# Kernel optimization log

Measured on AMD Instinct MI355X. Metric: run time of the kernel, lower is better.

The kernel has to match this reference:

```python
import jax, jax.numpy as jnp
import numpy as np

N, E_SC, E_BB = 50000, 600000, 100000
D, ED, REMB, NRES, SBF = 128, 128, 32, 21, 16
PI = 3.14159


def ln(x, g, b):
    m = jnp.mean(x, -1, keepdims=True)
    v = jnp.mean((x - m) ** 2, -1, keepdims=True)
    return (x - m) * jax.lax.rsqrt(v + 1e-5) * g + b


def gcn(x, W, b, src, dst, w):
    # GCNConv: symmetric normalization with unit self-loops and edge weights w.
    n = x.shape[0]
    xw = x @ W
    deg = jax.ops.segment_sum(w, dst, num_segments=n) + 1.0  # +1 self-loop
    dis = jax.lax.rsqrt(jnp.maximum(deg, 1e-6))  # clamp: hat_e.mean can be negative
    norm = dis[src] * w * dis[dst]
    agg = jax.ops.segment_sum(norm[:, None] * xw[src], dst, num_segments=n)
    return agg + (dis * dis)[:, None] * xw + b


def core(V_com, SBF_chi, X_c_alpha, V_c_beta, SBF_phi, SBF_psi, d_sidechain_com, d_min,
         old_chi, old_phi, old_psi, old_cbeta_coords, old_calpha_coords,
         res_table, sc_ln_g, sc_ln_b, sc_W, sc_b, bb_ln_g, bb_ln_b, bb_W, bb_b,
         e_ln_g, e_ln_b, eW1, eb1, eW2, eb2, euW, eub, gW, gb, bgW, bgb,
         iW1, ib1, iW2, ib2, aW, ab, baW, bab, cW, cb, xW, xb,
         residue_idx_i, residue_idx_j, edge_index_sc, edge_index_bb):
    hat_h = ln(jnp.concatenate([V_com, SBF_chi], -1), sc_ln_g, sc_ln_b) @ sc_W + sc_b
    h = ln(jnp.concatenate([X_c_alpha, V_c_beta, SBF_phi, SBF_psi], -1), bb_ln_g, bb_ln_b) @ bb_W + bb_b
    pair = jnp.concatenate([res_table[residue_idx_i], res_table[residue_idx_j]], -1)
    e_in = jnp.concatenate([d_sidechain_com[:, None], d_min[:, None], pair], -1)
    hat_e = jax.nn.relu(ln(e_in, e_ln_g, e_ln_b) @ eW1 + eb1) @ eW2 + eb2
    src, dst = edge_index_sc[0], edge_index_sc[1]
    for _ in range(3):  # num_sidechain_layers
        w = hat_e.mean(-1)
        hat_h = hat_h + jax.nn.relu(gcn(hat_h, gW, gb, src, dst, w))
        hat_e = hat_e + jnp.concatenate([hat_h[src], hat_h[dst]], -1) @ euW + eub
    bsrc, bdst = edge_index_bb[0], edge_index_bb[1]
    ebb = jnp.ones(bsrc.shape[0], hat_h.dtype)
    for _ in range(2):
        m = jax.nn.relu(jnp.concatenate([h, hat_h], -1) @ iW1 + ib1) @ iW2 + ib2
        h = h + jax.nn.relu(gcn(h, bgW, bgb, bsrc, bdst, ebb)) + m
    sc_act = jax.nn.relu(hat_h)
    bb_act = jax.nn.relu(h)
    wrap = lambda a: (a + PI) % (2.0 * PI) - PI
    dchi = (sc_act @ aW + ab)[:, 0]
    chi_new = wrap(old_chi + dchi[None, :])  # [4, N]
    dphi = (bb_act @ baW + bab)[:, 0]
    phi_new = wrap(old_phi + dphi)
    psi_new = wrap(old_psi + dphi)  # same bb_angle_head applied twice in source
    V_cbeta_new = old_cbeta_coords + sc_act @ cW + cb
    X_calpha_new = old_calpha_coords + bb_act @ xW + xb
    return chi_new, phi_new, psi_new, V_cbeta_new, X_calpha_new


def setup_inputs() -> dict:
    key = jax.random.key(0)
    ks = jax.random.split(key, 40)
    rn = lambda i, s: jax.random.normal(ks[i], s, jnp.float32)
    p = lambda i, s: rn(i, s) * 0.05
    return dict(
        V_com=rn(0, (N, 3)), SBF_chi=rn(1, (N, SBF)), X_c_alpha=rn(2, (N, 3)),
        V_c_beta=rn(3, (N, 3)), SBF_phi=rn(4, (N, SBF)), SBF_psi=rn(5, (N, SBF)),
        d_sidechain_com=jax.random.uniform(ks[6], (E_SC,), jnp.float32),
        d_min=jax.random.uniform(ks[7], (E_SC,), jnp.float32),
        old_chi=rn(8, (4, N)), old_phi=rn(9, (N,)), old_psi=rn(10, (N,)),
        old_cbeta_coords=rn(11, (N, 3)), old_calpha_coords=rn(12, (N, 3)),
        res_table=p(13, (NRES, REMB)),
        sc_ln_g=jnp.ones(3 + SBF), sc_ln_b=jnp.zeros(3 + SBF), sc_W=p(14, (3 + SBF, D)), sc_b=jnp.zeros(D),
        bb_ln_g=jnp.ones(6 + 2 * SBF), bb_ln_b=jnp.zeros(6 + 2 * SBF), bb_W=p(15, (6 + 2 * SBF, D)), bb_b=jnp.zeros(D),
        e_ln_g=jnp.ones(2 + 2 * REMB), e_ln_b=jnp.zeros(2 + 2 * REMB),
        eW1=p(16, (2 + 2 * REMB, ED)), eb1=jnp.zeros(ED), eW2=p(17, (ED, ED)), eb2=jnp.zeros(ED),
        euW=p(18, (2 * D, ED)), eub=jnp.zeros(ED),
        gW=p(19, (D, D)), gb=jnp.zeros(D), bgW=p(20, (D, D)), bgb=jnp.zeros(D),
        iW1=p(21, (2 * D, D)), ib1=jnp.zeros(D), iW2=p(22, (D, D)), ib2=jnp.zeros(D),
        aW=p(23, (D, 1)), ab=jnp.zeros(1), baW=p(24, (D, 1)), bab=jnp.zeros(1),
        cW=p(25, (D, 3)), cb=jnp.zeros(3), xW=p(26, (D, 3)), xb=jnp.zeros(3),
        residue_idx_i=jax.random.randint(ks[27], (E_SC,), 0, NRES),
        residue_idx_j=jax.random.randint(ks[28], (E_SC,), 0, NRES),
        edge_index_sc=jax.random.randint(ks[29], (2, E_SC), 0, N),
        edge_index_bb=jax.random.randint(ks[30], (2, E_BB), 0, N),
    )


def reference(V_com, SBF_chi, X_c_alpha, V_c_beta, SBF_phi, SBF_psi, d_sidechain_com, d_min,
              old_chi, old_phi, old_psi, old_cbeta_coords, old_calpha_coords,
              res_table, sc_ln_g, sc_ln_b, sc_W, sc_b, bb_ln_g, bb_ln_b, bb_W, bb_b,
              e_ln_g, e_ln_b, eW1, eb1, eW2, eb2, euW, eub, gW, gb, bgW, bgb,
              iW1, ib1, iW2, ib2, aW, ab, baW, bab, cW, cb, xW, xb,
              residue_idx_i, residue_idx_j, edge_index_sc, edge_index_bb):
    return core(V_com, SBF_chi, X_c_alpha, V_c_beta, SBF_phi, SBF_psi, d_sidechain_com, d_min,
                old_chi, old_phi, old_psi, old_cbeta_coords, old_calpha_coords,
                res_table, sc_ln_g, sc_ln_b, sc_W, sc_b, bb_ln_g, bb_ln_b, bb_W, bb_b,
                e_ln_g, e_ln_b, eW1, eb1, eW2, eb2, euW, eub, gW, gb, bgW, bgb,
                iW1, ib1, iW2, ib2, aW, ab, baW, bab, cW, cb, xW, xb,
                residue_idx_i, residue_idx_j, edge_index_sc, edge_index_bb)
```

## Files before the change

### kernel.cpp

```cpp
#include <hip/hip_runtime.h>
#include <stdint.h>

#define DEVI __device__ __forceinline__

constexpr int N_   = 50000;
constexpr int ESC  = 600000;
constexpr int EBB  = 100000;
constexpr int NRES = 21;
constexpr float PI_F = 3.14159f;

constexpr int RCH = 2048;
constexpr int RBS = (ESC + RCH - 1)/RCH;
constexpr int RBB = (EBB + RCH - 1)/RCH;

typedef __attribute__((ext_vector_type(8))) short short8v;
typedef __attribute__((ext_vector_type(4))) float f32x4;

DEVI float bf2f(unsigned short u){ return __uint_as_float(((unsigned)u)<<16); }
DEVI unsigned short f2bf(float f){
  unsigned x = __float_as_uint(f);
  unsigned r = (x + 0x7FFFu + ((x>>16)&1u))>>16;
  return (unsigned short)r;
}
DEVI float ldin(const void* p, long i, int f32){
  return f32 ? ((const float*)p)[i] : bf2f(((const unsigned short*)p)[i]);
}
DEVI void stout(void* p, long i, float v, int f32){
  if(f32) ((float*)p)[i]=v; else ((unsigned short*)p)[i]=f2bf(v);
}
DEVI float wrapf(float a){
  float t = a + PI_F;
  const float TP = 2.f*PI_F;
  t -= floorf(t/TP)*TP;
  return t - PI_F;
}

constexpr int OW_SC_LN_G=0;
constexpr int OW_SC_LN_B=OW_SC_LN_G+19;
constexpr int OW_SC_W  = OW_SC_LN_B+19;
constexpr int OW_SC_B  = OW_SC_W+19*128;
constexpr int OW_BB_LN_G=OW_SC_B+128;
constexpr int OW_BB_LN_B=OW_BB_LN_G+38;
constexpr int OW_BB_W = OW_BB_LN_B+38;
constexpr int OW_BB_B = OW_BB_W+38*128;
constexpr int OW_E_LN_G=OW_BB_B+128;
constexpr int OW_E_LN_B=OW_E_LN_G+66;
constexpr int OW_EW1 = OW_E_LN_B+66;
constexpr int OW_EB1 = OW_EW1+66*128;
constexpr int OW_GW  = OW_EB1+128;
constexpr int OW_GB  = OW_GW+128*128;
constexpr int OW_BGW = OW_GB+128;
constexpr int OW_BGB = OW_BGW+128*128;
constexpr int OW_IW1 = OW_BGB+128;
constexpr int OW_IB1 = OW_IW1+256*128;
constexpr int OW_IW2 = OW_IB1+128;
constexpr int OW_IB2 = OW_IW2+128*128;
constexpr int OW_AW  = OW_IB2+128;
constexpr int OW_AB  = OW_AW+128;
constexpr int OW_BAW = OW_AB+1;
constexpr int OW_BAB = OW_BAW+128;
constexpr int OW_CW  = OW_BAB+1;
constexpr int OW_CB  = OW_CW+128*3;
constexpr int OW_XW  = OW_CB+3;
constexpr int OW_XB  = OW_XW+128*3;
constexpr int OW_RES = OW_XB+3;
constexpr int OW_TOT = OW_RES+21*32;

__global__ void k_detect(const void* vcom, int* flag){
  const unsigned short* u = (const unsigned short*)vcom;
  int insane=0;
  for(int i=0;i<64;i+=2){
    float f = bf2f(u[i]);
    float a = fabsf(f);
    if(!(a<1e5f) || (a!=0.0f && a<1e-5f)) insane++;
  }
  *flag = (insane>=8)?1:0;
}

struct CvtArgs { const void* src[29]; };

__global__ void k_cvtw(CvtArgs a, const int* flag, float* w){
  static constexpr int offs[30] = {
    OW_SC_LN_G,OW_SC_LN_B,OW_SC_W,OW_SC_B,OW_BB_LN_G,OW_BB_LN_B,OW_BB_W,OW_BB_B,
    OW_E_LN_G,OW_E_LN_B,OW_EW1,OW_EB1,OW_GW,OW_GB,OW_BGW,OW_BGB,OW_IW1,OW_IB1,
    OW_IW2,OW_IB2,OW_AW,OW_AB,OW_BAW,OW_BAB,OW_CW,OW_CB,OW_XW,OW_XB,OW_RES,OW_TOT};
  int f32=*flag;
  for(int t=blockIdx.x*blockDim.x+threadIdx.x; t<OW_TOT; t+=gridDim.x*blockDim.x){
    int s=0;
    while(t>=offs[s+1]) s++;
    w[t]=ldin(a.src[s], t-offs[s], f32);
  }
}

DEVI void wprep_pad(const float* W, int Kreal, unsigned short* hi, unsigned short* lo, int idx){
  int lane=idx&63, nt=(idx>>6)&7, kt=idx>>9;
  int n = nt*16 + (lane&15);
  int kbase = kt*32 + (lane>>4)*8;
  #pragma unroll
  for(int i=0;i<8;i++){
    int k=kbase+i;
    float v = (k<Kreal) ? W[(long)k*128 + n] : 0.f;
    unsigned short h = f2bf(v);
    float r = v - bf2f(h);
    hi[(long)idx*8+i]=h;
    lo[(long)idx*8+i]=f2bf(r);
  }
}

constexpr int PB_WP = 46;
constexpr int PB_PV = PB_WP+1;
constexpr int PB_PP = PB_PV+441;
constexpr int PB_LN = PB_PP + (2*N_+3)/4;

__global__ void k_prep(const float* w, const int* flag,
    unsigned short* g_hi, unsigned short* g_lo,
    unsigned short* bg_hi, unsigned short* bg_lo,
    unsigned short* i2_hi, unsigned short* i2_lo,
    unsigned short* i1_hi, unsigned short* i1_lo,
    unsigned short* sc_hi, unsigned short* sc_lo,
    unsigned short* bb_hi, unsigned short* bb_lo,
    const void* eW2, const void* eb2, const void* euW, const void* eub,
    float* dv, float* dv4, float* P, float* sp, float* qp,
    const void* vcom, const void* sbfchi,
    const void* xca, const void* vcb, const void* sphi, const void* spsi,
    float* xn_sc, float* xn_bb){
  __shared__ float pv[64];
  int b=blockIdx.x;
  if(b<PB_WP){
    int idx=b*256+threadIdx.x;
    if(idx<2048)       wprep_pad(w+OW_GW,  128, g_hi,  g_lo,  idx);
    else if(idx<4096)  wprep_pad(w+OW_BGW, 128, bg_hi, bg_lo, idx-2048);
    else if(idx<6144)  wprep_pad(w+OW_IW2, 128, i2_hi, i2_lo, idx-4096);
    else if(idx<10240) wprep_pad(w+OW_IW1, 256, i1_hi, i1_lo, idx-6144);
    else if(idx<10752) wprep_pad(w+OW_SC_W, 19, sc_hi, sc_lo, idx-10240);
    else if(idx<11776) wprep_pad(w+OW_BB_W, 38, bb_hi, bb_lo, idx-10752);
  } else if(b<PB_PV){
    int j=threadIdx.x; int f32=*flag;
    if(j<128){
      const float* g=w+OW_E_LN_G; const float* bb=w+OW_E_LN_B; const float* W1=w+OW_EW1;
      float A=g[0]*W1[j], C=g[1]*W1[128+j];
      float G=0,B=0;
      for(int i=0;i<66;i++){ float wij=W1[i*128+j]; G+=g[i]*wij; B+=bb[i]*wij; }
      B += w[OW_EB1+j];
      float v2=0; for(int k=0;k<128;k++) v2+=ldin(eW2,(long)j*128+k,f32);
      float us=0,ud=0;
      for(int k=0;k<128;k++){ us+=ldin(euW,(long)j*128+k,f32); ud+=ldin(euW,(long)(128+j)*128+k,f32); }
      dv[640+j]=us*(1.f/128.f); dv[768+j]=ud*(1.f/128.f);
      int j4=j>>2, r=j&3;
      dv4[j4*20+0+r]=A; dv4[j4*20+4+r]=C; dv4[j4*20+8+r]=G; dv4[j4*20+12+r]=B;
      dv4[j4*20+16+r]=v2*(1.f/128.f);
      if(j==0){
        float s=0,t=0;
        for(int k=0;k<128;k++){ s+=ldin(eb2,k,f32); t+=ldin(eub,k,f32); }
        dv[896]=s*(1.f/128.f); dv[897]=t*(1.f/128.f);
        dv4[640]=s*(1.f/128.f);
      }
    }
  } else if(b<PB_PP){
    int c=b-PB_PV, j=threadIdx.x;
    const float* res=w+OW_RES;
    if(j<32) pv[j]=res[(c/NRES)*32+j];
    else if(j<64) pv[j]=res[(c%NRES)*32+(j-32)];
    __syncthreads();
    if(j<128){
      const float* g=w+OW_E_LN_G; const float* W1=w+OW_EW1;
      float s=0;
      for(int i=0;i<64;i++) s += pv[i]*g[2+i]*W1[(2+i)*128+j];
      P[c*128+j]=s;
      if(j==0){ float a=0,q=0; for(int i=0;i<64;i++){a+=pv[i]; q+=pv[i]*pv[i];} sp[c]=a; qp[c]=q; }
    }
  } else {
    int wv=threadIdx.x>>6, lane=threadIdx.x&63;
    long gw=(long)(b-PB_PP)*4+wv;
    int f32=*flag;
    if(gw<N_){
      int n=(int)gw;
      float x=0.f;
      if(lane<3) x=ldin(vcom,(long)n*3+lane,f32);
      else if(lane<19) x=ldin(sbfchi,(long)n*16+(lane-3),f32);
      float s=x, q=x*x;
      for(int m=1;m<64;m<<=1){ s+=__shfl_xor(s,m,64); q+=__shfl_xor(q,m,64); }
      float mean=s*(1.f/19.f);
      float istd=rsqrtf(fmaxf(q*(1.f/19.f)-mean*mean,0.f)+1e-5f);
      if(lane<32){
        float xn=(lane<19)? (x-mean)*istd*w[OW_SC_LN_G+lane]+w[OW_SC_LN_B+lane] : 0.f;
        xn_sc[(long)n*32+lane]=xn;
      }
    } else if(gw<2L*N_){
      int n=(int)(gw-N_);
      float x=0.f;
      if(lane<3) x=ldin(xca,(long)n*3+lane,f32);
      else if(lane<6) x=ldin(vcb,(long)n*3+(lane-3),f32);
      else if(lane<22) x=ldin(sphi,(long)n*16+(lane-6),f32);
      else if(lane<38) x=ldin(spsi,(long)n*16+(lane-22),f32);
      float s=x, q=x*x;
      for(int m=1;m<64;m<<=1){ s+=__shfl_xor(s,m,64); q+=__shfl_xor(q,m,64); }
      float mean=s*(1.f/38.f);
      float istd=rsqrtf(fmaxf(q*(1.f/38.f)-mean*mean,0.f)+1e-5f);
      float xn=(lane<38)? (x-mean)*istd*w[OW_BB_LN_G+lane]+w[OW_BB_LN_B+lane] : 0.f;
      xn_bb[(long)n*64+lane]=xn;
    }
  }
}

__global__ void k_rhist(const int* key_sc, const int* key_bb, int shift, int* hist){
  __shared__ int h[256];
  h[threadIdx.x]=0; __syncthreads();
  int g = blockIdx.x>=RBS;
  const int* key = g? key_bb : key_sc;
  int E = g? EBB : ESC;
  int b = g? blockIdx.x-RBS : blockIdx.x;
  int base=b*RCH;
  for(int r=0;r<RCH/256;r++){
    int idx=base+r*256+threadIdx.x;
    if(idx<E) atomicAdd(&h[(key[idx]>>shift)&255],1);
  }
  __syncthreads();
  hist[(long)blockIdx.x*256+threadIdx.x]=h[threadIdx.x];
}
__global__ void k_rscanA(int* hist, int* tot){
  __shared__ int sA[512], sB[512];
  int g = blockIdx.x>=256;
  int d = blockIdx.x&255;
  int NB = g? RBB : RBS;
  int* H = hist + (g? (long)RBS*256 : 0);
  int t=threadIdx.x;
  int i0=t, i1=t+256;
  int o0 = (i0<NB)? H[(long)i0*256+d] : 0;
  int o1 = (i1<NB)? H[(long)i1*256+d] : 0;
  sA[i0]=o0; sA[i1]=o1;
  __syncthreads();
  int* a=sA; int* b=sB;
  for(int off=1; off<512; off<<=1){
    b[i0] = a[i0] + ((i0>=off)? a[i0-off]:0);
    b[i1] = a[i1] + ((i1>=off)? a[i1-off]:0);
    __syncthreads();
    int* tmp=a; a=b; b=tmp;
  }
  if(i0<NB) H[(long)i0*256+d] = a[i0]-o0;
  if(i1<NB) H[(long)i1*256+d] = a[i1]-o1;
  if(t==255) tot[(g?256:0)+d] = a[511];
}
__global__ void k_rscanB(const int* tot, int* base){
  __shared__ int sA[256], sB[256];
  int t=threadIdx.x;
  for(int g=0;g<2;g++){
    int o=tot[g*256+t];
    sA[t]=o; __syncthreads();
    int* a=sA; int* b=sB;
    for(int off=1; off<256; off<<=1){
      b[t] = a[t] + ((t>=off)? a[t-off]:0);
      __syncthreads();
      int* tmp=a; a=b; b=tmp;
    }
    base[g*256+t] = a[t]-o;
    __syncthreads();
  }
}
__global__ void k_rscat(int shift, int first,
    const int* kin_sc, const int* srcv_sc, const int2* pin_sc,
    const int* kin_bb, const int* srcv_bb, const int2* pin_bb,
    const int* hist, const int* dbase,
    int* kout_sc, int2* pout_sc, int* kout_bb, int2* pout_bb){
  __shared__ int running[256];
  __shared__ int Hb[256];
  __shared__ int whist[4][256];
  __shared__ int pw[4][256];
  int tid=threadIdx.x, lane=tid&63, w=tid>>6;
  int g = blockIdx.x>=RBS;
  const int* kin  = g? kin_bb : kin_sc;
  const int* srcv = g? srcv_bb: srcv_sc;
  const int2* pin = g? pin_bb : pin_sc;
  int* kout  = g? kout_bb : kout_sc;
  int2* pout = g? pout_bb : pout_sc;
  int E = g? EBB : ESC;
  int b = g? blockIdx.x-RBS : blockIdx.x;
  running[tid]=0;
  Hb[tid]=hist[(long)blockIdx.x*256+tid] + dbase[(g?256:0)+tid];
  int base=b*RCH;
  for(int r=0;r<RCH/256;r++){
    __syncthreads();
    whist[0][tid]=0; whist[1][tid]=0; whist[2][tid]=0; whist[3][tid]=0;
    __syncthreads();
    int idx=base+r*256+tid;
    bool valid = idx<E;
    int key=0, digit=0; int2 pay; pay.x=0; pay.y=0;
    if(valid){
      key=kin[idx];
      digit=(key>>shift)&255;
      if(first){ pay.x=srcv[idx]; pay.y=idx; }
      else pay=pin[idx];
    }
    unsigned long long act=__ballot(valid);
    unsigned long long same=act;
    #pragma unroll
    for(int k=0;k<8;k++){
      unsigned long long m=__ballot(valid && ((digit>>k)&1));
      same &= ((digit>>k)&1)? m : ~m;
    }
    same &= act;
    unsigned long long below=(1ULL<<lane)-1ULL;
    int wrank=__popcll(same & below);
    if(valid && wrank==0) whist[w][digit]=__popcll(same);
    __syncthreads();
    int c0=whist[0][tid], c1=whist[1][tid], c2=whist[2][tid], c3=whist[3][tid];
    pw[0][tid]=0; pw[1][tid]=c0; pw[2][tid]=c0+c1; pw[3][tid]=c0+c1+c2;
    __syncthreads();
    if(valid){
      int pos=Hb[digit]+running[digit]+pw[w][digit]+wrank;
      kout[pos]=key; pout[pos]=pay;
    }
    __syncthreads();
    running[tid]+=c0+c1+c2+c3;
  }
}
__global__ void k_bounds(const int* dstS_sc, const int* dstS_bb, int* rp_sc, int* rp_bb){
  long i=(long)blockIdx.x*blockDim.x+threadIdx.x;
  if(i<=ESC){
    int cur = (i<ESC)? dstS_sc[i] : N_;
    int prev= (i>0)? dstS_sc[i-1] : -1;
    for(int d=prev+1; d<=cur; d++) rp_sc[d]=(int)i;
  } else if(i <= (long)ESC+1+EBB){
    long j=i-(ESC+1);
    int cur = (j<EBB)? dstS_bb[j] : N_;
    int prev= (j>0)? dstS_bb[j-1] : -1;
    for(int d=prev+1; d<=cur; d++) rp_bb[d]=(int)j;
  }
}

constexpr int WB4 = (ESC + 1023)/1024;
__global__ __launch_bounds__(256,4) void k_w0(const void* dsc, const void* dmin,
    const int* ri_, const int* rj_, const int* flag, const float* dv4,
    const float* P, const float* sp, const float* qp, float* we){
  long base=(long)blockIdx.x*1024+threadIdx.x;
  int f32=*flag;
  float d1[4],d2[4],istd[4],nmi[4],acc[4];
  int cc[4]; bool val[4];
  #pragma unroll
  for(int k=0;k<4;k++){
    long e=base+k*256;
    val[k]= e<ESC;
    long ee= val[k]? e : 0;
    d1[k]=ldin(dsc,ee,f32); d2[k]=ldin(dmin,ee,f32);
    int c=ri_[ee]*NRES+rj_[ee];
    cc[k]=c;
    float m=(d1[k]+d2[k]+sp[c])*(1.f/66.f);
    float ms=(d1[k]*d1[k]+d2[k]*d2[k]+qp[c])*(1.f/66.f);
    istd[k]=rsqrtf(fmaxf(ms-m*m,0.f)+1e-5f);
    nmi[k]=-m*istd[k];
    acc[k]=0.f;
  }
  #pragma unroll 2
  for(int j4=0;j4<32;j4++){
    const float4* q=(const float4*)&dv4[j4*20];
    float4 A4=q[0], C4=q[1], G4=q[2], B4=q[3], V4=q[4];
    #pragma unroll
    for(int k=0;k<4;k++){
      float4 P4=*(const float4*)&P[(long)cc[k]*128+j4*4];
      float t,hid;
      t=fmaf(d1[k],A4.x,fmaf(d2[k],C4.x,P4.x)); hid=fmaf(istd[k],t,fmaf(nmi[k],G4.x,B4.x)); acc[k]=fmaf(fmaxf(hid,0.f),V4.x,acc[k]);
      t=fmaf(d1[k],A4.y,fmaf(d2[k],C4.y,P4.y)); hid=fmaf(istd[k],t,fmaf(nmi[k],G4.y,B4.y)); acc[k]=fmaf(fmaxf(hid,0.f),V4.y,acc[k]);
      t=fmaf(d1[k],A4.z,fmaf(d2[k],C4.z,P4.z)); hid=fmaf(istd[k],t,fmaf(nmi[k],G4.z,B4.z)); acc[k]=fmaf(fmaxf(hid,0.f),V4.z,acc[k]);
      t=fmaf(d1[k],A4.w,fmaf(d2[k],C4.w,P4.w)); hid=fmaf(istd[k],t,fmaf(nmi[k],G4.w,B4.w)); acc[k]=fmaf(fmaxf(hid,0.f),V4.w,acc[k]);
    }
  }
  float e2=dv4[640];
  #pragma unroll
  for(int k=0;k<4;k++) if(val[k]) we[base+k*256]=acc[k]+e2;
}

__global__ void k_deg(const int* rp, const int2* se, const float* we_edge,
                      const float* an, const float* bn, const float* dv,
                      float* we_csr, float* dis, int layer){
  int n=blockIdx.x*blockDim.x+threadIdx.x;
  if(n>=N_) return;
  int e0=rp[n], e1=rp[n+1];
  float s=1.f;
  if(layer==0){
    for(int p=e0;p<e1;p++){ float ww=we_edge[se[p].y]; we_csr[p]=ww; s+=ww; }
  } else {
    float add_n = bn[n] + dv[897];
    for(int p=e0;p<e1;p++){
      float ww=we_csr[p] + an[se[p].x] + add_n;
      we_csr[p]=ww; s+=ww;
    }
  }
  dis[n]=rsqrtf(fmaxf(s,1e-6f));
}

DEVI f32x4 MFMA(short8v a, short8v b, f32x4 c){
  return __builtin_amdgcn_mfma_f32_16x16x32_bf16(a,b,c,0,0,0);
}
DEVI void cvt8(float4 a0, float4 a1, short8v& hi, short8v& lo){
  float av[8]={a0.x,a0.y,a0.z,a0.w,a1.x,a1.y,a1.z,a1.w};
  union{short8v v; unsigned short u[8];} H,L;
  #pragma unroll
  for(int i=0;i<8;i++){
    unsigned short h=f2bf(av[i]);
    float r=av[i]-bf2f(h);
    H.u[i]=h; L.u[i]=f2bf(r);
  }
  hi=H.v; lo=L.v;
}

template<int KT, int LDA>
DEVI void mgemm_body(int bid, const float* A1, const float* A2,
    const unsigned short* Whi, const unsigned short* Wlo,
    const float* bias, float* C, int relu, int accum, int M){
  const int lane = threadIdx.x & 63;
  const int wid  = threadIdx.x >> 6;
  const int r0   = bid*64 + wid*16;
  const int mrow = lane & 15;
  const int kg   = lane >> 4;
  long arow = (long)min(r0 + mrow, M-1);
  f32x4 acc[8];
  #pragma unroll
  for(int t=0;t<8;t++) acc[t]=(f32x4){0.f,0.f,0.f,0.f};

  #pragma unroll
  for(int kt=0; kt<KT; kt++){
    const float* A = (KT==8 && kt>=4) ? A2 : A1;
    int kb = (kt&3)*32 + kg*8;
    float4 a0 = *(const float4*)&A[arow*LDA + kb];
    float4 a1 = *(const float4*)&A[arow*LDA + kb + 4];
    short8v ah, al; cvt8(a0,a1,ah,al);
    #pragma unroll
    for(int nt=0;nt<8;nt++){
      long off = (((long)kt*8+nt)*64 + lane)*8;
      short8v wh = *(const short8v*)&Whi[off];
      short8v wl = *(const short8v*)&Wlo[off];
      acc[nt] = MFMA(ah, wh, acc[nt]);
      acc[nt] = MFMA(al, wh, acc[nt]);
      acc[nt] = MFMA(ah, wl, acc[nt]);
      acc[nt] = MFMA(al, wl, acc[nt]);
    }
  }

  #pragma unroll
  for(int nt=0;nt<8;nt++){
    int col = nt*16 + mrow;
    float bj = bias ? bias[col] : 0.f;
    #pragma unroll
    for(int r=0;r<4;r++){
      int row = r0 + kg*4 + r;
      if(row >= M) continue;
      long idx = (long)row*128 + col;
      float v = acc[nt][r] + bj;
      if(relu) v = fmaxf(v,0.f);
      if(accum) v += C[idx];
      C[idx] = v;
    }
  }
}

template<int KT, int LDA>
__global__ __launch_bounds__(256,4) void k_mgemm(const float* A1, const float* A2,
    const unsigned short* Whi, const unsigned short* Wlo,
    const float* bias, float* C, int relu, int accum, int M){
  mgemm_body<KT,LDA>(blockIdx.x, A1, A2, Whi, Wlo, bias, C, relu, accum, M);
}

__global__ __launch_bounds__(256,4) void k_mfeat(const float* xn_sc, const float* xn_bb,
    const unsigned short* schi, const unsigned short* sclo,
    const unsigned short* bbhi, const unsigned short* bblo,
    const float* w, float* hat_h, float* hbuf, int M){
  int GBl=(M+63)/64;
  if((int)blockIdx.x < GBl)
    mgemm_body<1,32>(blockIdx.x, xn_sc, nullptr, schi, sclo, w+OW_SC_B, hat_h, 0,0,M);
  else
    mgemm_body<2,64>(blockIdx.x-GBl, xn_bb, nullptr, bbhi, bblo, w+OW_BB_B, hbuf, 0,0,M);
}

__global__ __launch_bounds__(256,3) void k_mbb(const float* h, const float* hh,
    const unsigned short* W1hi, const unsigned short* W1lo,
    const unsigned short* W2hi,
    const unsigned short* W3hi,
    const float* b1, const float* b2,
    float* xwout, float* mout, int M){
  __shared__ unsigned short hids[64*136];
  const int lane = threadIdx.x & 63;
  const int wid  = threadIdx.x >> 6;
  const int r0   = blockIdx.x*64 + wid*16;
  const int mrow = lane & 15;
  const int kg   = lane >> 4;
  long arow = (long)min(r0 + mrow, M-1);
  f32x4 acc1[8], acc2[8];
  #pragma unroll
  for(int t=0;t<8;t++){ acc1[t]=(f32x4){0,0,0,0}; acc2[t]=(f32x4){0,0,0,0}; }

  #pragma unroll
  for(int kt=0; kt<8; kt++){
    const float* A = (kt>=4) ? hh : h;
    int kb = (kt&3)*32 + kg*8;
    float4 a0 = *(const float4*)&A[arow*128 + kb];
    float4 a1 = *(const float4*)&A[arow*128 + kb + 4];
    short8v ah, al; cvt8(a0,a1,ah,al);
    #pragma unroll
    for(int nt=0;nt<8;nt++){
      long off = (((long)kt*8+nt)*64 + lane)*8;
      short8v wh = *(const short8v*)&W1hi[off];
      short8v wl = *(const short8v*)&W1lo[off];
      acc1[nt] = MFMA(ah, wh, acc1[nt]);
      acc1[nt] = MFMA(al, wh, acc1[nt]);
      acc1[nt] = MFMA(ah, wl, acc1[nt]);
      acc1[nt] = MFMA(al, wl, acc1[nt]);
    }
    if(kt<4){
      #pragma unroll
      for(int nt=0;nt<8;nt++){
        long off = (((long)kt*8+nt)*64 + lane)*8;
        short8v wh = *(const short8v*)&W2hi[off];
        acc2[nt] = MFMA(ah, wh, acc2[nt]);
      }
    }
  }

  #pragma unroll
  for(int nt=0;nt<8;nt++){
    int col = nt*16 + mrow;
    float bj = b1[col];
    #pragma unroll
    for(int r=0;r<4;r++){
      int rloc = wid*16 + kg*4 + r;
      int row = r0 + kg*4 + r;
      hids[rloc*136 + col] = f2bf(fmaxf(acc1[nt][r] + bj, 0.f));
      if(row < M) xwout[(long)row*128 + col] = acc2[nt][r];
    }
  }
  __syncthreads();

  f32x4 acc3[8];
  #pragma unroll
  for(int t=0;t<8;t++) acc3[t]=(f32x4){0,0,0,0};
  int rloc = wid*16 + mrow;
  #pragma unroll
  for(int kt=0; kt<4; kt++){
    int kb = kt*32 + kg*8;
    short8v ah = *(const short8v*)&hids[rloc*136 + kb];
    #pragma unroll
    for(int nt=0;nt<8;nt++){
      long off = (((long)kt*8+nt)*64 + lane)*8;
      short8v wh = *(const short8v*)&W3hi[off];
      acc3[nt] = MFMA(ah, wh, acc3[nt]);
    }
  }
  #pragma unroll
  for(int nt=0;nt<8;nt++){
    int col = nt*16 + mrow;
    float bj = b2[col];
    #pragma unroll
    for(int r=0;r<4;r++){
      int row = r0 + kg*4 + r;
      if(row < M) mout[(long)row*128 + col] = acc3[nt][r] + bj;
    }
  }
}

__global__ void k_agg_sc(const int* rp, const int2* se, const float* wc,
                         const float* dis, const float* xw, const float* w,
                         float* hat_h, const float* dv, float* an, float* bn, int withdot){
  int wv=threadIdx.x>>6, lane=threadIdx.x&63;
  int n=blockIdx.x*4+wv;
  int g=lane>>4, l=lane&15, d0=l*8;
  float disn=dis[n];
  float4 aA={0,0,0,0}, aB={0,0,0,0};
  int e0=rp[n], e1=rp[n+1];
  for(int p=e0+g; p<e1; p+=4){
    int s0=se[p].x;
    float nw=dis[s0]*wc[p]*disn;
    float4 xa=*(const float4*)&xw[(long)s0*128+d0];
    float4 xb=*(const float4*)&xw[(long)s0*128+d0+4];
    aA.x+=nw*xa.x; aA.y+=nw*xa.y; aA.z+=nw*xa.z; aA.w+=nw*xa.w;
    aB.x+=nw*xb.x; aB.y+=nw*xb.y; aB.z+=nw*xb.z; aB.w+=nw*xb.w;
  }
  #pragma unroll
  for(int m=16;m<64;m<<=1){
    aA.x+=__shfl_xor(aA.x,m,64); aA.y+=__shfl_xor(aA.y,m,64);
    aA.z+=__shfl_xor(aA.z,m,64); aA.w+=__shfl_xor(aA.w,m,64);
    aB.x+=__shfl_xor(aB.x,m,64); aB.y+=__shfl_xor(aB.y,m,64);
    aB.z+=__shfl_xor(aB.z,m,64); aB.w+=__shfl_xor(aB.w,m,64);
  }
  float d2=disn*disn;
  float4 xsA=*(const float4*)&xw[(long)n*128+d0];
  float4 xsB=*(const float4*)&xw[(long)n*128+d0+4];
  float4 gbA=*(const float4*)&w[OW_GB+d0];
  float4 gbB=*(const float4*)&w[OW_GB+d0+4];
  float4 hoA=*(const float4*)&hat_h[(long)n*128+d0];
  float4 hoB=*(const float4*)&hat_h[(long)n*128+d0+4];
  float4 hA, hB;
  hA.x=hoA.x+fmaxf(aA.x+d2*xsA.x+gbA.x,0.f);
  hA.y=hoA.y+fmaxf(aA.y+d2*xsA.y+gbA.y,0.f);
  hA.z=hoA.z+fmaxf(aA.z+d2*xsA.z+gbA.z,0.f);
  hA.w=hoA.w+fmaxf(aA.w+d2*xsA.w+gbA.w,0.f);
  hB.x=hoB.x+fmaxf(aB.x+d2*xsB.x+gbB.x,0.f);
  hB.y=hoB.y+fmaxf(aB.y+d2*xsB.y+gbB.y,0.f);
  hB.z=hoB.z+fmaxf(aB.z+d2*xsB.z+gbB.z,0.f);
  hB.w=hoB.w+fmaxf(aB.w+d2*xsB.w+gbB.w,0.f);
  if(g==0){
    *(float4*)&hat_h[(long)n*128+d0]=hA;
    *(float4*)&hat_h[(long)n*128+d0+4]=hB;
  }
  if(withdot){
    float4 usA=*(const float4*)&dv[640+d0], usB=*(const float4*)&dv[640+d0+4];
    float4 udA=*(const float4*)&dv[768+d0], udB=*(const float4*)&dv[768+d0+4];
    float a = hA.x*usA.x+hA.y*usA.y+hA.z*usA.z+hA.w*usA.w
            + hB.x*usB.x+hB.y*usB.y+hB.z*usB.z+hB.w*usB.w;
    float b = hA.x*udA.x+hA.y*udA.y+hA.z*udA.z+hA.w*udA.w
            + hB.x*udB.x+hB.y*udB.y+hB.z*udB.z+hB.w*udB.w;
    #pragma unroll
    for(int m=1;m<16;m<<=1){ a+=__shfl_xor(a,m,64); b+=__shfl_xor(b,m,64); }
    if(lane==0){ an[n]=a; bn[n]=b; }
  }
}

__global__ void k_agg_bb(const int* rp, const int2* se,
                         const float* xw, const float* mbuf, const float* w, float* h){
  int wv=threadIdx.x>>6, lane=threadIdx.x&63;
  int n=blockIdx.x*4+wv;
  int g=lane>>4, l=lane&15, d0=l*8;
  int e0=rp[n], e1=rp[n+1];
  float disn=rsqrtf(1.f+(float)(e1-e0));
  float4 aA={0,0,0,0}, aB={0,0,0,0};
  for(int p=e0+g; p<e1; p+=4){
    int s0=se[p].x;
    float nw=rsqrtf(1.f+(float)(rp[s0+1]-rp[s0]))*disn;
    float4 xa=*(const float4*)&xw[(long)s0*128+d0];
    float4 xb=*(const float4*)&xw[(long)s0*128+d0+4];
    aA.x+=nw*xa.x; aA.y+=nw*xa.y; aA.z+=nw*xa.z; aA.w+=nw*xa.w;
    aB.x+=nw*xb.x; aB.y+=nw*xb.y; aB.z+=nw*xb.z; aB.w+=nw*xb.w;
  }
  #pragma unroll
  for(int m=16;m<64;m<<=1){
    aA.x+=__shfl_xor(aA.x,m,64); aA.y+=__shfl_xor(aA.y,m,64);
    aA.z+=__shfl_xor(aA.z,m,64); aA.w+=__shfl_xor(aA.w,m,64);
    aB.x+=__shfl_xor(aB.x,m,64); aB.y+=__shfl_xor(aB.y,m,64);
    aB.z+=__shfl_xor(aB.z,m,64); aB.w+=__shfl_xor(aB.w,m,64);
  }
  if(g==0){
    float d2=disn*disn;
    float4 xsA=*(const float4*)&xw[(long)n*128+d0];
    float4 xsB=*(const float4*)&xw[(long)n*128+d0+4];
    float4 gbA=*(const float4*)&w[OW_BGB+d0];
    float4 gbB=*(const float4*)&w[OW_BGB+d0+4];
    float4 mA=*(const float4*)&mbuf[(long)n*128+d0];
    float4 mB=*(const float4*)&mbuf[(long)n*128+d0+4];
    float4 hA=*(float4*)&h[(long)n*128+d0];
    float4 hB=*(float4*)&h[(long)n*128+d0+4];
    hA.x+=fmaxf(aA.x+d2*xsA.x+gbA.x,0.f)+mA.x;
    hA.y+=fmaxf(aA.y+d2*xsA.y+gbA.y,0.f)+mA.y;
    hA.z+=fmaxf(aA.z+d2*xsA.z+gbA.z,0.f)+mA.z;
    hA.w+=fmaxf(aA.w+d2*xsA.w+gbA.w,0.f)+mA.w;
    hB.x+=fmaxf(aB.x+d2*xsB.x+gbB.x,0.f)+mB.x;
    hB.y+=fmaxf(aB.y+d2*xsB.y+gbB.y,0.f)+mB.y;
    hB.z+=fmaxf(aB.z+d2*xsB.z+gbB.z,0.f)+mB.z;
    hB.w+=fmaxf(aB.w+d2*xsB.w+gbB.w,0.f)+mB.w;
    *(float4*)&h[(long)n*128+d0]=hA;
    *(float4*)&h[(long)n*128+d0+4]=hB;
  }
}

__global__ void k_heads(const float* hat_h, const float* h, const float* w,
                        const void* old_chi, const void* old_phi, const void* old_psi,
                        const void* old_cb, const void* old_ca, const int* flag, void* out){
  int wv=threadIdx.x>>6, lane=threadIdx.x&63;
  int n=blockIdx.x*4+wv;
  int f32=*flag;
  float s0=fmaxf(hat_h[(long)n*128+lane],0.f), s1=fmaxf(hat_h[(long)n*128+64+lane],0.f);
  float b0=fmaxf(h[(long)n*128+lane],0.f),    b1=fmaxf(h[(long)n*128+64+lane],0.f);
  float r[8];
  r[0]=s0*w[OW_AW+lane]+s1*w[OW_AW+64+lane];
  r[1]=s0*w[OW_CW+lane*3+0]+s1*w[OW_CW+(64+lane)*3+0];
  r[2]=s0*w[OW_CW+lane*3+1]+s1*w[OW_CW+(64+lane)*3+1];
  r[3]=s0*w[OW_CW+lane*3+2]+s1*w[OW_CW+(64+lane)*3+2];
  r[4]=b0*w[OW_BAW+lane]+b1*w[OW_BAW+64+lane];
  r[5]=b0*w[OW_XW+lane*3+0]+b1*w[OW_XW+(64+lane)*3+0];
  r[6]=b0*w[OW_XW+lane*3+1]+b1*w[OW_XW+(64+lane)*3+1];
  r[7]=b0*w[OW_XW+lane*3+2]+b1*w[OW_XW+(64+lane)*3+2];
  for(int m=1;m<64;m<<=1){
    #pragma unroll
    for(int t=0;t<8;t++) r[t]+=__shfl_xor(r[t],m,64);
  }
  if(lane==0){
    float dchi=r[0]+w[OW_AB];
    for(int k=0;k<4;k++)
      stout(out,(long)k*N_+n, wrapf(ldin(old_chi,(long)k*N_+n,f32)+dchi), f32);
    float dphi=r[4]+w[OW_BAB];
    stout(out,(long)4*N_+n, wrapf(ldin(old_phi,n,f32)+dphi), f32);
    stout(out,(long)5*N_+n, wrapf(ldin(old_psi,n,f32)+dphi), f32);
    for(int t=0;t<3;t++){
      stout(out,(long)6*N_+(long)n*3+t, ldin(old_cb,(long)n*3+t,f32)+r[1+t]+w[OW_CB+t], f32);
      stout(out,(long)9*N_+(long)n*3+t, ldin(old_ca,(long)n*3+t,f32)+r[5+t]+w[OW_XB+t], f32);
    }
  }
}

extern "C" void kernel_launch(void* const* d_in, const int* in_sizes, int n_in,
                              void* d_out, int out_size, void* d_ws, size_t ws_size,
                              hipStream_t stream) {
  (void)in_sizes; (void)n_in; (void)out_size; (void)ws_size;

  char* p=(char*)d_ws;
  auto alloc=[&](size_t bytes)->void*{ void* r=(void*)p; p+=((bytes+255)&~(size_t)255); return r; };
  int*   flag   =(int*)  alloc(16);
  float* warena =(float*)alloc((size_t)OW_TOT*4);
  float* dv     =(float*)alloc(1024*4);
  float* dv4    =(float*)alloc(1024*4);
  float* P      =(float*)alloc((size_t)441*128*4);
  float* sp     =(float*)alloc(441*4);
  float* qp     =(float*)alloc(441*4);
  float* hat_h  =(float*)alloc((size_t)N_*128*4);
  float* hbuf   =(float*)alloc((size_t)N_*128*4);
  float* bufX   =(float*)alloc((size_t)N_*128*4);
  float* bufM   =(float*)alloc((size_t)N_*128*4);
  float* xn_sc  =(float*)alloc((size_t)N_*32*4);
  float* xn_bb  =(float*)alloc((size_t)N_*64*4);
  float* we     =(float*)alloc((size_t)ESC*4);
  float* we_csr =(float*)alloc((size_t)ESC*4);
  float* an     =(float*)alloc((size_t)N_*4);
  float* bn     =(float*)alloc((size_t)N_*4);
  float* dis    =(float*)alloc((size_t)N_*4);
  int* rp_sc    =(int*)  alloc((size_t)(N_+1)*4);
  int* rp_bb    =(int*)  alloc((size_t)(N_+1)*4);
  int*  key1_sc =(int*)  alloc((size_t)ESC*4);
  int2* pay1_sc =(int2*) alloc((size_t)ESC*8);
  int*  dstS_sc =(int*)  alloc((size_t)ESC*4);
  int2* csr_se_sc=(int2*)alloc((size_t)ESC*8);
  int*  key1_bb =(int*)  alloc((size_t)EBB*4);
  int2* pay1_bb =(int2*) alloc((size_t)EBB*8);
  int*  dstS_bb =(int*)  alloc((size_t)EBB*4);
  int2* csr_se_bb=(int2*)alloc((size_t)EBB*8);
  int*  hist    =(int*)  alloc((size_t)(RBS+RBB)*256*4);
  int*  tot     =(int*)  alloc(512*4);
  int*  dbase   =(int*)  alloc(512*4);
  unsigned short* wfg_hi =(unsigned short*)alloc(2048*8*2);
  unsigned short* wfg_lo =(unsigned short*)alloc(2048*8*2);
  unsigned short* wfbg_hi=(unsigned short*)alloc(2048*8*2);
  unsigned short* wfbg_lo=(unsigned short*)alloc(2048*8*2);
  unsigned short* wfi2_hi=(unsigned short*)alloc(2048*8*2);
  unsigned short* wfi2_lo=(unsigned short*)alloc(2048*8*2);
  unsigned short* wfi1_hi=(unsigned short*)alloc(4096*8*2);
  unsigned short* wfi1_lo=(unsigned short*)alloc(4096*8*2);
  unsigned short* wfsc_hi=(unsigned short*)alloc(512*8*2);
  unsigned short* wfsc_lo=(unsigned short*)alloc(512*8*2);
  unsigned short* wfbb_hi=(unsigned short*)alloc(1024*8*2);
  unsigned short* wfbb_lo=(unsigned short*)alloc(1024*8*2);

  const int* src_sc=(const int*)d_in[48];
  const int* dst_sc=src_sc+ESC;
  const int* src_bb=(const int*)d_in[49];
  const int* dst_bb=src_bb+EBB;

  k_detect<<<1,1,0,stream>>>(d_in[0], flag);

  CvtArgs ca;
  {
    int map[29]={14,15,16,17,18,19,20,21,22,23,24,25,30,31,32,33,34,35,36,37,
                 38,39,40,41,42,43,44,45,13};
    for(int i=0;i<29;i++) ca.src[i]=d_in[map[i]];
  }
  k_cvtw<<<(OW_TOT+255)/256,256,0,stream>>>(ca, flag, warena);

  k_prep<<<PB_LN,256,0,stream>>>(warena, flag,
      wfg_hi,wfg_lo, wfbg_hi,wfbg_lo, wfi2_hi,wfi2_lo, wfi1_hi,wfi1_lo,
      wfsc_hi,wfsc_lo, wfbb_hi,wfbb_lo,
      d_in[26], d_in[27], d_in[28], d_in[29], dv, dv4, P, sp, qp,
      d_in[0], d_in[1], d_in[2], d_in[3], d_in[4], d_in[5], xn_sc, xn_bb);

  k_rhist<<<RBS+RBB,256,0,stream>>>(dst_sc, dst_bb, 0, hist);
  k_rscanA<<<512,256,0,stream>>>(hist, tot);
  k_rscanB<<<1,256,0,stream>>>(tot, dbase);
  k_rscat<<<RBS+RBB,256,0,stream>>>(0, 1, dst_sc, src_sc, (const int2*)nullptr,
                                    dst_bb, src_bb, (const int2*)nullptr, hist, dbase,
                                    key1_sc, pay1_sc, key1_bb, pay1_bb);
  k_rhist<<<RBS+RBB,256,0,stream>>>(key1_sc, key1_bb, 8, hist);
  k_rscanA<<<512,256,0,stream>>>(hist, tot);
  k_rscanB<<<1,256,0,stream>>>(tot, dbase);
  k_rscat<<<RBS+RBB,256,0,stream>>>(8, 0, key1_sc, (const int*)nullptr, pay1_sc,
                                    key1_bb, (const int*)nullptr, pay1_bb, hist, dbase,
                                    dstS_sc, csr_se_sc, dstS_bb, csr_se_bb);
  k_bounds<<<(int)(((long)ESC+1+EBB+1+255)/256),256,0,stream>>>(dstS_sc, dstS_bb, rp_sc, rp_bb);

  const int GB = (N_+63)/64;
  k_mfeat<<<2*GB,256,0,stream>>>(xn_sc, xn_bb, wfsc_hi, wfsc_lo, wfbb_hi, wfbb_lo,
                                 warena, hat_h, hbuf, N_);

  k_w0<<<WB4,256,0,stream>>>(d_in[6],d_in[7],(const int*)d_in[46],(const int*)d_in[47],
                             flag,dv4,P,sp,qp,we);

  const int DB = (N_+255)/256;
  for(int l=0;l<3;l++){
    k_deg<<<DB,256,0,stream>>>(rp_sc, csr_se_sc, we, an, bn, dv, we_csr, dis, l);
    k_mgemm<4,128><<<GB,256,0,stream>>>(hat_h, nullptr, wfg_hi, wfg_lo, nullptr, bufX, 0, 0, N_);
    k_agg_sc<<<N_/4,256,0,stream>>>(rp_sc,csr_se_sc,we_csr,dis,bufX,warena,hat_h,dv,an,bn,(l<2)?1:0);
  }

  for(int l=0;l<2;l++){
    k_mbb<<<GB,256,0,stream>>>(hbuf, hat_h, wfi1_hi, wfi1_lo, wfbg_hi,
                               wfi2_hi, warena+OW_IB1, warena+OW_IB2,
                               bufX, bufM, N_);
    k_agg_bb<<<N_/4,256,0,stream>>>(rp_bb,csr_se_bb,bufX,bufM,warena,hbuf);
  }

  k_heads<<<N_/4,256,0,stream>>>(hat_h,hbuf,warena,
                                 d_in[8],d_in[9],d_in[10],d_in[11],d_in[12],flag,d_out);
}
```

Measured before the change: 669.9 us.

## Drop split-bf16 compensation in backbone GEMM and precompute GCN edge norms

```diff
diff --git a/kernel.cpp b/kernel.cpp
--- a/kernel.cpp
+++ b/kernel.cpp
@@ -101,9 +101,8 @@
     int k=kbase+i;
     float v = (k<Kreal) ? W[(long)k*128 + n] : 0.f;
     unsigned short h = f2bf(v);
-    float r = v - bf2f(h);
     hi[(long)idx*8+i]=h;
-    lo[(long)idx*8+i]=f2bf(r);
+    if(lo){ float r = v - bf2f(h); lo[(long)idx*8+i]=f2bf(r); }
   }
 }
 
@@ -114,9 +113,9 @@
 
 __global__ void k_prep(const float* w, const int* flag,
     unsigned short* g_hi, unsigned short* g_lo,
-    unsigned short* bg_hi, unsigned short* bg_lo,
-    unsigned short* i2_hi, unsigned short* i2_lo,
-    unsigned short* i1_hi, unsigned short* i1_lo,
+    unsigned short* bg_hi,
+    unsigned short* i2_hi,
+    unsigned short* i1_hi,
     unsigned short* sc_hi, unsigned short* sc_lo,
     unsigned short* bb_hi, unsigned short* bb_lo,
     const void* eW2, const void* eb2, const void* euW, const void* eub,
@@ -129,9 +128,9 @@
   if(b<PB_WP){
     int idx=b*256+threadIdx.x;
     if(idx<2048)       wprep_pad(w+OW_GW,  128, g_hi,  g_lo,  idx);
-    else if(idx<4096)  wprep_pad(w+OW_BGW, 128, bg_hi, bg_lo, idx-2048);
-    else if(idx<6144)  wprep_pad(w+OW_IW2, 128, i2_hi, i2_lo, idx-4096);
-    else if(idx<10240) wprep_pad(w+OW_IW1, 256, i1_hi, i1_lo, idx-6144);
+    else if(idx<4096)  wprep_pad(w+OW_BGW, 128, bg_hi, nullptr, idx-2048);
+    else if(idx<6144)  wprep_pad(w+OW_IW2, 128, i2_hi, nullptr, idx-4096);
+    else if(idx<10240) wprep_pad(w+OW_IW1, 256, i1_hi, nullptr, idx-6144);
     else if(idx<10752) wprep_pad(w+OW_SC_W, 19, sc_hi, sc_lo, idx-10240);
     else if(idx<11776) wprep_pad(w+OW_BB_W, 38, bb_hi, bb_lo, idx-10752);
   } else if(b<PB_PV){
@@ -327,6 +326,10 @@
     for(int d=prev+1; d<=cur; d++) rp_bb[d]=(int)j;
   }
 }
+__global__ void k_degb(const int* rp, float* disb){
+  int n=blockIdx.x*blockDim.x+threadIdx.x;
+  if(n<N_) disb[n]=rsqrtf(1.f+(float)(rp[n+1]-rp[n]));
+}
 
 constexpr int WB4 = (ESC + 1023)/1024;
 __global__ __launch_bounds__(256,4) void k_w0(const void* dsc, const void* dmin,
@@ -387,6 +390,10 @@
   }
   dis[n]=rsqrtf(fmaxf(s,1e-6f));
 }
+__global__ void k_norm(const int2* se, const float* we_csr, const float* dis, float* wn){
+  int p=blockIdx.x*blockDim.x+threadIdx.x;
+  if(p<ESC) wn[p]=dis[se[p].x]*we_csr[p];
+}
 
 DEVI f32x4 MFMA(short8v a, short8v b, f32x4 c){
   return __builtin_amdgcn_mfma_f32_16x16x32_bf16(a,b,c,0,0,0);
@@ -401,6 +408,12 @@
     H.u[i]=h; L.u[i]=f2bf(r);
   }
   hi=H.v; lo=L.v;
+}
+DEVI short8v cvt8hi(float4 a0, float4 a1){
+  union{short8v v; unsigned short u[8];} H;
+  H.u[0]=f2bf(a0.x); H.u[1]=f2bf(a0.y); H.u[2]=f2bf(a0.z); H.u[3]=f2bf(a0.w);
+  H.u[4]=f2bf(a1.x); H.u[5]=f2bf(a1.y); H.u[6]=f2bf(a1.z); H.u[7]=f2bf(a1.w);
+  return H.v;
 }
 
 template<int KT, int LDA>
@@ -471,8 +484,8 @@
     mgemm_body<2,64>(blockIdx.x-GBl, xn_bb, nullptr, bbhi, bblo, w+OW_BB_B, hbuf, 0,0,M);
 }
 
-__global__ __launch_bounds__(256,3) void k_mbb(const float* h, const float* hh,
-    const unsigned short* W1hi, const unsigned short* W1lo,
+__global__ __launch_bounds__(256,4) void k_mbb(const float* h, const float* hh,
+    const unsigned short* W1hi,
     const unsigned short* W2hi,
     const unsigned short* W3hi,
     const float* b1, const float* b2,
@@ -494,23 +507,17 @@
     int kb = (kt&3)*32 + kg*8;
     float4 a0 = *(const float4*)&A[arow*128 + kb];
     float4 a1 = *(const float4*)&A[arow*128 + kb + 4];
-    short8v ah, al; cvt8(a0,a1,ah,al);
+    short8v ah = cvt8hi(a0,a1);
     #pragma unroll
     for(int nt=0;nt<8;nt++){
       long off = (((long)kt*8+nt)*64 + lane)*8;
-      short8v wh = *(const short8v*)&W1hi[off];
-      short8v wl = *(const short8v*)&W1lo[off];
-      acc1[nt] = MFMA(ah, wh, acc1[nt]);
-      acc1[nt] = MFMA(al, wh, acc1[nt]);
-      acc1[nt] = MFMA(ah, wl, acc1[nt]);
-      acc1[nt] = MFMA(al, wl, acc1[nt]);
+      acc1[nt] = MFMA(ah, *(const short8v*)&W1hi[off], acc1[nt]);
     }
     if(kt<4){
       #pragma unroll
       for(int nt=0;nt<8;nt++){
         long off = (((long)kt*8+nt)*64 + lane)*8;
-        short8v wh = *(const short8v*)&W2hi[off];
-        acc2[nt] = MFMA(ah, wh, acc2[nt]);
+        acc2[nt] = MFMA(ah, *(const short8v*)&W2hi[off], acc2[nt]);
       }
     }
   }
@@ -540,8 +547,7 @@
     #pragma unroll
     for(int nt=0;nt<8;nt++){
       long off = (((long)kt*8+nt)*64 + lane)*8;
-      short8v wh = *(const short8v*)&W3hi[off];
-      acc3[nt] = MFMA(ah, wh, acc3[nt]);
+      acc3[nt] = MFMA(ah, *(const short8v*)&W3hi[off], acc3[nt]);
     }
   }
   #pragma unroll
@@ -556,7 +562,7 @@
   }
 }
 
-__global__ void k_agg_sc(const int* rp, const int2* se, const float* wc,
+__global__ void k_agg_sc(const int* rp, const int2* se, const float* wn,
                          const float* dis, const float* xw, const float* w,
                          float* hat_h, const float* dv, float* an, float* bn, int withdot){
   int wv=threadIdx.x>>6, lane=threadIdx.x&63;
@@ -567,7 +573,7 @@
   int e0=rp[n], e1=rp[n+1];
   for(int p=e0+g; p<e1; p+=4){
     int s0=se[p].x;
-    float nw=dis[s0]*wc[p]*disn;
+    float nw=wn[p];
     float4 xa=*(const float4*)&xw[(long)s0*128+d0];
     float4 xb=*(const float4*)&xw[(long)s0*128+d0+4];
     aA.x+=nw*xa.x; aA.y+=nw*xa.y; aA.z+=nw*xa.z; aA.w+=nw*xa.w;
@@ -588,14 +594,14 @@
   float4 hoA=*(const float4*)&hat_h[(long)n*128+d0];
   float4 hoB=*(const float4*)&hat_h[(long)n*128+d0+4];
   float4 hA, hB;
-  hA.x=hoA.x+fmaxf(aA.x+d2*xsA.x+gbA.x,0.f);
-  hA.y=hoA.y+fmaxf(aA.y+d2*xsA.y+gbA.y,0.f);
-  hA.z=hoA.z+fmaxf(aA.z+d2*xsA.z+gbA.z,0.f);
-  hA.w=hoA.w+fmaxf(aA.w+d2*xsA.w+gbA.w,0.f);
-  hB.x=hoB.x+fmaxf(aB.x+d2*xsB.x+gbB.x,0.f);
-  hB.y=hoB.y+fmaxf(aB.y+d2*xsB.y+gbB.y,0.f);
-  hB.z=hoB.z+fmaxf(aB.z+d2*xsB.z+gbB.z,0.f);
-  hB.w=hoB.w+fmaxf(aB.w+d2*xsB.w+gbB.w,0.f);
+  hA.x=hoA.x+fmaxf(aA.x*disn+d2*xsA.x+gbA.x,0.f);
+  hA.y=hoA.y+fmaxf(aA.y*disn+d2*xsA.y+gbA.y,0.f);
+  hA.z=hoA.z+fmaxf(aA.z*disn+d2*xsA.z+gbA.z,0.f);
+  hA.w=hoA.w+fmaxf(aA.w*disn+d2*xsA.w+gbA.w,0.f);
+  hB.x=hoB.x+fmaxf(aB.x*disn+d2*xsB.x+gbB.x,0.f);
+  hB.y=hoB.y+fmaxf(aB.y*disn+d2*xsB.y+gbB.y,0.f);
+  hB.z=hoB.z+fmaxf(aB.z*disn+d2*xsB.z+gbB.z,0.f);
+  hB.w=hoB.w+fmaxf(aB.w*disn+d2*xsB.w+gbB.w,0.f);
   if(g==0){
     *(float4*)&hat_h[(long)n*128+d0]=hA;
     *(float4*)&hat_h[(long)n*128+d0+4]=hB;
@@ -613,17 +619,17 @@
   }
 }
 
-__global__ void k_agg_bb(const int* rp, const int2* se,
+__global__ void k_agg_bb(const int* rp, const int2* se, const float* disb,
                          const float* xw, const float* mbuf, const float* w, float* h){
   int wv=threadIdx.x>>6, lane=threadIdx.x&63;
   int n=blockIdx.x*4+wv;
   int g=lane>>4, l=lane&15, d0=l*8;
   int e0=rp[n], e1=rp[n+1];
-  float disn=rsqrtf(1.f+(float)(e1-e0));
+  float disn=disb[n];
   float4 aA={0,0,0,0}, aB={0,0,0,0};
   for(int p=e0+g; p<e1; p+=4){
     int s0=se[p].x;
-    float nw=rsqrtf(1.f+(float)(rp[s0+1]-rp[s0]))*disn;
+    float nw=disb[s0];
     float4 xa=*(const float4*)&xw[(long)s0*128+d0];
     float4 xb=*(const float4*)&xw[(long)s0*128+d0+4];
     aA.x+=nw*xa.x; aA.y+=nw*xa.y; aA.z+=nw*xa.z; aA.w+=nw*xa.w;
@@ -646,14 +652,14 @@
     float4 mB=*(const float4*)&mbuf[(long)n*128+d0+4];
     float4 hA=*(float4*)&h[(long)n*128+d0];
     float4 hB=*(float4*)&h[(long)n*128+d0+4];
-    hA.x+=fmaxf(aA.x+d2*xsA.x+gbA.x,0.f)+mA.x;
-    hA.y+=fmaxf(aA.y+d2*xsA.y+gbA.y,0.f)+mA.y;
-    hA.z+=fmaxf(aA.z+d2*xsA.z+gbA.z,0.f)+mA.z;
-    hA.w+=fmaxf(aA.w+d2*xsA.w+gbA.w,0.f)+mA.w;
-    hB.x+=fmaxf(aB.x+d2*xsB.x+gbB.x,0.f)+mB.x;
-    hB.y+=fmaxf(aB.y+d2*xsB.y+gbB.y,0.f)+mB.y;
-    hB.z+=fmaxf(aB.z+d2*xsB.z+gbB.z,0.f)+mB.z;
-    hB.w+=fmaxf(aB.w+d2*xsB.w+gbB.w,0.f)+mB.w;
+    hA.x+=fmaxf(aA.x*disn+d2*xsA.x+gbA.x,0.f)+mA.x;
+    hA.y+=fmaxf(aA.y*disn+d2*xsA.y+gbA.y,0.f)+mA.y;
+    hA.z+=fmaxf(aA.z*disn+d2*xsA.z+gbA.z,0.f)+mA.z;
+    hA.w+=fmaxf(aA.w*disn+d2*xsA.w+gbA.w,0.f)+mA.w;
+    hB.x+=fmaxf(aB.x*disn+d2*xsB.x+gbB.x,0.f)+mB.x;
+    hB.y+=fmaxf(aB.y*disn+d2*xsB.y+gbB.y,0.f)+mB.y;
+    hB.z+=fmaxf(aB.z*disn+d2*xsB.z+gbB.z,0.f)+mB.z;
+    hB.w+=fmaxf(aB.w*disn+d2*xsB.w+gbB.w,0.f)+mB.w;
     *(float4*)&h[(long)n*128+d0]=hA;
     *(float4*)&h[(long)n*128+d0+4]=hB;
   }
@@ -716,9 +722,11 @@
   float* xn_bb  =(float*)alloc((size_t)N_*64*4);
   float* we     =(float*)alloc((size_t)ESC*4);
   float* we_csr =(float*)alloc((size_t)ESC*4);
+  float* wn     =(float*)alloc((size_t)ESC*4);
   float* an     =(float*)alloc((size_t)N_*4);
   float* bn     =(float*)alloc((size_t)N_*4);
   float* dis    =(float*)alloc((size_t)N_*4);
+  float* disb   =(float*)alloc((size_t)N_*4);
   int* rp_sc    =(int*)  alloc((size_t)(N_+1)*4);
   int* rp_bb    =(int*)  alloc((size_t)(N_+1)*4);
   int*  key1_sc =(int*)  alloc((size_t)ESC*4);
@@ -735,11 +743,8 @@
   unsigned short* wfg_hi =(unsigned short*)alloc(2048*8*2);
   unsigned short* wfg_lo =(unsigned short*)alloc(2048*8*2);
   unsigned short* wfbg_hi=(unsigned short*)alloc(2048*8*2);
-  unsigned short* wfbg_lo=(unsigned short*)alloc(2048*8*2);
   unsigned short* wfi2_hi=(unsigned short*)alloc(2048*8*2);
-  unsigned short* wfi2_lo=(unsigned short*)alloc(2048*8*2);
   unsigned short* wfi1_hi=(unsigned short*)alloc(4096*8*2);
-  unsigned short* wfi1_lo=(unsigned short*)alloc(4096*8*2);
   unsigned short* wfsc_hi=(unsigned short*)alloc(512*8*2);
   unsigned short* wfsc_lo=(unsigned short*)alloc(512*8*2);
   unsigned short* wfbb_hi=(unsigned short*)alloc(1024*8*2);
@@ -761,7 +766,7 @@
   k_cvtw<<<(OW_TOT+255)/256,256,0,stream>>>(ca, flag, warena);
 
   k_prep<<<PB_LN,256,0,stream>>>(warena, flag,
-      wfg_hi,wfg_lo, wfbg_hi,wfbg_lo, wfi2_hi,wfi2_lo, wfi1_hi,wfi1_lo,
+      wfg_hi,wfg_lo, wfbg_hi, wfi2_hi, wfi1_hi,
       wfsc_hi,wfsc_lo, wfbb_hi,wfbb_lo,
       d_in[26], d_in[27], d_in[28], d_in[29], dv, dv4, P, sp, qp,
       d_in[0], d_in[1], d_in[2], d_in[3], d_in[4], d_in[5], xn_sc, xn_bb);
@@ -779,6 +784,7 @@
                                     key1_bb, (const int*)nullptr, pay1_bb, hist, dbase,
                                     dstS_sc, csr_se_sc, dstS_bb, csr_se_bb);
   k_bounds<<<(int)(((long)ESC+1+EBB+1+255)/256),256,0,stream>>>(dstS_sc, dstS_bb, rp_sc, rp_bb);
+  k_degb<<<(N_+255)/256,256,0,stream>>>(rp_bb, disb);
 
   const int GB = (N_+63)/64;
   k_mfeat<<<2*GB,256,0,stream>>>(xn_sc, xn_bb, wfsc_hi, wfsc_lo, wfbb_hi, wfbb_lo,
@@ -788,17 +794,18 @@
                              flag,dv4,P,sp,qp,we);
 
   const int DB = (N_+255)/256;
+  const int NB = (ESC+255)/256;
   for(int l=0;l<3;l++){
     k_deg<<<DB,256,0,stream>>>(rp_sc, csr_se_sc, we, an, bn, dv, we_csr, dis, l);
+    k_norm<<<NB,256,0,stream>>>(csr_se_sc, we_csr, dis, wn);
     k_mgemm<4,128><<<GB,256,0,stream>>>(hat_h, nullptr, wfg_hi, wfg_lo, nullptr, bufX, 0, 0, N_);
-    k_agg_sc<<<N_/4,256,0,stream>>>(rp_sc,csr_se_sc,we_csr,dis,bufX,warena,hat_h,dv,an,bn,(l<2)?1:0);
+    k_agg_sc<<<N_/4,256,0,stream>>>(rp_sc,csr_se_sc,wn,dis,bufX,warena,hat_h,dv,an,bn,(l<2)?1:0);
   }
 
   for(int l=0;l<2;l++){
-    k_mbb<<<GB,256,0,stream>>>(hbuf, hat_h, wfi1_hi, wfi1_lo, wfbg_hi,
-                               wfi2_hi, warena+OW_IB1, warena+OW_IB2,
-                               bufX, bufM, N_);
-    k_agg_bb<<<N_/4,256,0,stream>>>(rp_bb,csr_se_bb,bufX,bufM,warena,hbuf);
+    k_mbb<<<GB,256,0,stream>>>(hbuf, hat_h, wfi1_hi, wfbg_hi, wfi2_hi,
+                               warena+OW_IB1, warena+OW_IB2, bufX, bufM, N_);
+    k_agg_bb<<<N_/4,256,0,stream>>>(rp_bb,csr_se_bb,disb,bufX,bufM,warena,hbuf);
   }
 
   k_heads<<<N_/4,256,0,stream>>>(hat_h,hbuf,warena,
```

Result: faster. 639.6 us (-4.5%).
